# Performance work log

Hardware: AMD Instinct MI355X
Metric: run time of the kernel (lower is better)

Reference implementation:

```python
import jax, jax.numpy as jnp
import numpy as np

OUT_HW = 224  # fixed by the dilation tensor built inside forward
K = 3         # kernel size


def _axis_terms(coords, size):
    """Bilinear interpolation terms along one axis.
    coords: float coordinates, any shape. Returns clipped int neighbor
    indices (i0, i1) and weights (w0, w1) with zero weight outside [0, size)."""
    c0 = jnp.floor(coords)
    f = coords - c0
    i0 = c0.astype(jnp.int32)
    i1 = i0 + 1
    w0 = (1.0 - f) * ((i0 >= 0) & (i0 < size)).astype(coords.dtype)
    w1 = f * ((i1 >= 0) & (i1 < size)).astype(coords.dtype)
    return jnp.clip(i0, 0, size - 1), jnp.clip(i1, 0, size - 1), w0, w1


def setup_inputs() -> dict:
    key = jax.random.key(0)
    k1, k2, k3 = jax.random.split(key, 3)
    B, C, H, W = 16, 3, 1024, 1024
    x = jax.random.normal(k1, (B, C, H, W), dtype=jnp.float32)
    # normalized sample coordinates in [-1, 1] per output row / column
    stride_h = jax.random.uniform(k2, (B, OUT_HW), dtype=jnp.float32, minval=-1.0, maxval=1.0)
    stride_w = jax.random.uniform(k3, (B, OUT_HW), dtype=jnp.float32, minval=-1.0, maxval=1.0)
    # fixed identity weight from __init__: center tap on channel diagonal
    w = np.zeros((3, 3, K, K), dtype=np.float32)
    for c in range(3):
        w[c, c, 1, 1] = 1.0
    return {"x": x, "stride_h": stride_h, "stride_w": stride_w, "weight": jnp.asarray(w)}


def reference(x, stride_h, stride_w, weight):
    B, C, H, W = x.shape
    dt = x.dtype
    # map normalized [-1,1] coords to pixel coords (as in forward)
    ch = (stride_h + 1.0) * (H - 1) * 0.5            # [B, outH]
    cw = (stride_w + 1.0) * (W - 1) * 0.5            # [B, outW]
    offs = (jnp.arange(K, dtype=dt) - (K - 1) / 2)   # dilation == 1 (built as ones in forward)
    ys = ch[:, :, None] + offs                       # [B, outH, K]
    xs = cw[:, :, None] + offs                       # [B, outW, K]

    yi0, yi1, wy0, wy1 = _axis_terms(ys, H)
    xi0, xi1, wx0, wx1 = _axis_terms(xs, W)

    # gather rows: [B, C, outH, K, W]
    gat_h = jax.vmap(lambda xb, idx: xb[:, idx, :])
    row = (wy0[:, None, :, :, None] * gat_h(x, yi0)
           + wy1[:, None, :, :, None] * gat_h(x, yi1))
    # gather cols: [B, C, outH, Kh, outW, Kw]
    gat_w = jax.vmap(lambda rb, idx: rb[..., idx])
    samp = (wx0[:, None, None, None] * gat_w(row, xi0)
            + wx1[:, None, None, None] * gat_w(row, xi1))
    # contract with (fixed) kernel: out[b,o,i,j]
    return jnp.einsum('bciujv,ocuv->boij', samp, weight)
```

## Files before the change

### kernel.cpp

```cpp
#include <hip/hip_runtime.h>

#define OH 224
#define OW 224
#define HH 1024
#define WW 1024

typedef float f4u __attribute__((ext_vector_type(4), aligned(4)));

__global__ __launch_bounds__(256) void adaptive_sam_kernel(
    const float* __restrict__ x,
    const float* __restrict__ sh,
    const float* __restrict__ sw,
    const float* __restrict__ wgt,
    float* __restrict__ out,
    int B)
{
    __shared__ float ws[81];
    if (threadIdx.x < 81) ws[threadIdx.x] = wgt[threadIdx.x];
    __syncthreads();

    int site = blockIdx.x * blockDim.x + threadIdx.x;
    const int total = B * OH * OW;
    if (site >= total) return;

    int j = site % OW;
    int t = site / OW;
    int i = t % OH;
    int b = t / OH;

    float chf = (sh[b * OH + i] + 1.0f) * ((HH - 1) * 0.5f);
    float cwf = (sw[b * OW + j] + 1.0f) * ((WW - 1) * 0.5f);
    float cyf = floorf(chf); float fy = chf - cyf; int iy = (int)cyf;
    float cxf = floorf(cwf); float fx = cwf - cxf; int ix = (int)cxf;

    int rb = min(max(iy - 1, 0), HH - 4);
    int cb = min(max(ix - 1, 0), WW - 4);

    float Wy[3][4], Wx[3][4];
    #pragma unroll
    for (int u = 0; u < 3; ++u) {
        int y0 = iy + u - 1, y1 = y0 + 1;
        float a0 = (1.0f - fy) * ((y0 >= 0 && y0 < HH) ? 1.0f : 0.0f);
        float a1 = fy          * ((y1 >= 0 && y1 < HH) ? 1.0f : 0.0f);
        int py0 = min(max(y0, 0), HH - 1) - rb;
        int py1 = min(max(y1, 0), HH - 1) - rb;

        int x0 = ix + u - 1, x1 = x0 + 1;
        float b0 = (1.0f - fx) * ((x0 >= 0 && x0 < WW) ? 1.0f : 0.0f);
        float b1 = fx          * ((x1 >= 0 && x1 < WW) ? 1.0f : 0.0f);
        int px0 = min(max(x0, 0), WW - 1) - cb;
        int px1 = min(max(x1, 0), WW - 1) - cb;

        #pragma unroll
        for (int p = 0; p < 4; ++p) {
            Wy[u][p] = (py0 == p ? a0 : 0.0f) + (py1 == p ? a1 : 0.0f);
            Wx[u][p] = (px0 == p ? b0 : 0.0f) + (px1 == p ? b1 : 0.0f);
        }
    }

    float acc0 = 0.0f, acc1 = 0.0f, acc2 = 0.0f;
    const float* xb = x + (size_t)b * 3 * HH * WW;

    #pragma unroll
    for (int c = 0; c < 3; ++c) {
        const float* pr = xb + (size_t)c * HH * WW + (size_t)rb * WW + cb;
        f4u q0 = *reinterpret_cast<const f4u*>(pr);
        f4u q1 = *reinterpret_cast<const f4u*>(pr + WW);
        f4u q2 = *reinterpret_cast<const f4u*>(pr + 2 * WW);
        f4u q3 = *reinterpret_cast<const f4u*>(pr + 3 * WW);

        float hx[4][3];
        #pragma unroll
        for (int v = 0; v < 3; ++v) {
            hx[0][v] = Wx[v][0]*q0.x + Wx[v][1]*q0.y + Wx[v][2]*q0.z + Wx[v][3]*q0.w;
            hx[1][v] = Wx[v][0]*q1.x + Wx[v][1]*q1.y + Wx[v][2]*q1.z + Wx[v][3]*q1.w;
            hx[2][v] = Wx[v][0]*q2.x + Wx[v][1]*q2.y + Wx[v][2]*q2.z + Wx[v][3]*q2.w;
            hx[3][v] = Wx[v][0]*q3.x + Wx[v][1]*q3.y + Wx[v][2]*q3.z + Wx[v][3]*q3.w;
        }
        #pragma unroll
        for (int u = 0; u < 3; ++u)
            #pragma unroll
            for (int v = 0; v < 3; ++v) {
                float s = Wy[u][0]*hx[0][v] + Wy[u][1]*hx[1][v]
                        + Wy[u][2]*hx[2][v] + Wy[u][3]*hx[3][v];
                int wi = c * 9 + u * 3 + v;
                acc0 = fmaf(ws[wi],      s, acc0);
                acc1 = fmaf(ws[27 + wi], s, acc1);
                acc2 = fmaf(ws[54 + wi], s, acc2);
            }
    }

    size_t obase = (size_t)b * 3 * OH * OW + (size_t)i * OW + j;
    out[obase]               = acc0;
    out[obase + OH * OW]     = acc1;
    out[obase + 2 * OH * OW] = acc2;
}

extern "C" void kernel_launch(void* const* d_in, const int* in_sizes, int n_in,
                              void* d_out, int out_size, void* d_ws, size_t ws_size,
                              hipStream_t stream) {
    const float* x  = (const float*)d_in[0];
    const float* sh = (const float*)d_in[1];
    const float* sw = (const float*)d_in[2];
    const float* w  = (const float*)d_in[3];
    float* out = (float*)d_out;

    int B = in_sizes[1] / OH;
    int total = B * OH * OW;
    dim3 grid((total + 255) / 256);
    adaptive_sam_kernel<<<grid, 256, 0, stream>>>(x, sh, sw, w, out, B);
}
```

Baseline: 266.5 us.

## Stage four input rows per output row into LDS with async global_load_lds

The kernel now launches one block per (batch, output row). Each block copies the four needed input rows for all three channels into shared memory, 48KB, using coalesced 16-byte global_load_lds transfers. Threads then read their 4x4 neighbourhoods from LDS instead of doing scattered unaligned global float4 gathers. The aim is to turn random sub-line accesses into streaming contiguous loads. In exchange it always fetches full rows, even columns no thread uses, and the large LDS footprint limits how many blocks fit on a CU, with no overlap between the load and compute phases inside a block.

```diff
diff --git a/kernel.cpp b/kernel.cpp
--- a/kernel.cpp
+++ b/kernel.cpp
@@ -4,8 +4,10 @@
 #define OW 224
 #define HH 1024
 #define WW 1024
+#define HW (HH * WW)
 
-typedef float f4u __attribute__((ext_vector_type(4), aligned(4)));
+typedef __attribute__((address_space(3))) void lds_void_t;
+typedef const __attribute__((address_space(1))) void g_void_t;
 
 __global__ __launch_bounds__(256) void adaptive_sam_kernel(
     const float* __restrict__ x,
@@ -15,85 +17,97 @@
     float* __restrict__ out,
     int B)
 {
+    __shared__ float lds[3 * 4 * WW];
     __shared__ float ws[81];
-    if (threadIdx.x < 81) ws[threadIdx.x] = wgt[threadIdx.x];
+
+    const int tid = threadIdx.x;
+    const int bi  = blockIdx.x;
+    const int i   = bi % OH;
+    const int b   = bi / OH;
+
+    if (tid < 81) ws[tid] = wgt[tid];
+
+    float chf = (sh[b * OH + i] + 1.0f) * ((HH - 1) * 0.5f);
+    float cyf = floorf(chf); float fy = chf - cyf; int iy = (int)cyf;
+    int rb = min(max(iy - 1, 0), HH - 4);
+
+    {
+        const int lane = tid & 63;
+        const int wv   = tid >> 6;
+        #pragma unroll
+        for (int c = 0; c < 3; ++c) {
+            const float* gbase = x + (size_t)(b * 3 + c) * HW + (size_t)rb * WW + wv * 1024;
+            float* lbase = &lds[c * 4096 + wv * 1024];
+            #pragma unroll
+            for (int n = 0; n < 4; ++n) {
+                const float* gp = gbase + n * 256 + lane * 4;
+                __builtin_amdgcn_global_load_lds((g_void_t*)gp,
+                                                 (lds_void_t*)(lbase + n * 256),
+                                                 16, 0, 0);
+            }
+        }
+    }
     __syncthreads();
 
-    int site = blockIdx.x * blockDim.x + threadIdx.x;
-    const int total = B * OH * OW;
-    if (site >= total) return;
+    if (tid < OW) {
+        const int j = tid;
+        float cwf = (sw[b * OW + j] + 1.0f) * ((WW - 1) * 0.5f);
+        float cxf = floorf(cwf); float fx = cwf - cxf; int ix = (int)cxf;
+        int cb = min(max(ix - 1, 0), WW - 4);
 
-    int j = site % OW;
-    int t = site / OW;
-    int i = t % OH;
-    int b = t / OH;
+        float Wy[3][4], Wx[3][4];
+        #pragma unroll
+        for (int u = 0; u < 3; ++u) {
+            int y0 = iy + u - 1, y1 = y0 + 1;
+            float a0 = (1.0f - fy) * ((y0 >= 0 && y0 < HH) ? 1.0f : 0.0f);
+            float a1 = fy          * ((y1 >= 0 && y1 < HH) ? 1.0f : 0.0f);
+            int py0 = min(max(y0, 0), HH - 1) - rb;
+            int py1 = min(max(y1, 0), HH - 1) - rb;
 
-    float chf = (sh[b * OH + i] + 1.0f) * ((HH - 1) * 0.5f);
-    float cwf = (sw[b * OW + j] + 1.0f) * ((WW - 1) * 0.5f);
-    float cyf = floorf(chf); float fy = chf - cyf; int iy = (int)cyf;
-    float cxf = floorf(cwf); float fx = cwf - cxf; int ix = (int)cxf;
+            int x0 = ix + u - 1, x1 = x0 + 1;
+            float b0 = (1.0f - fx) * ((x0 >= 0 && x0 < WW) ? 1.0f : 0.0f);
+            float b1 = fx          * ((x1 >= 0 && x1 < WW) ? 1.0f : 0.0f);
+            int px0 = min(max(x0, 0), WW - 1) - cb;
+            int px1 = min(max(x1, 0), WW - 1) - cb;
 
-    int rb = min(max(iy - 1, 0), HH - 4);
-    int cb = min(max(ix - 1, 0), WW - 4);
+            #pragma unroll
+            for (int p = 0; p < 4; ++p) {
+                Wy[u][p] = (py0 == p ? a0 : 0.0f) + (py1 == p ? a1 : 0.0f);
+                Wx[u][p] = (px0 == p ? b0 : 0.0f) + (px1 == p ? b1 : 0.0f);
+            }
+        }
 
-    float Wy[3][4], Wx[3][4];
-    #pragma unroll
-    for (int u = 0; u < 3; ++u) {
-        int y0 = iy + u - 1, y1 = y0 + 1;
-        float a0 = (1.0f - fy) * ((y0 >= 0 && y0 < HH) ? 1.0f : 0.0f);
-        float a1 = fy          * ((y1 >= 0 && y1 < HH) ? 1.0f : 0.0f);
-        int py0 = min(max(y0, 0), HH - 1) - rb;
-        int py1 = min(max(y1, 0), HH - 1) - rb;
+        float acc0 = 0.0f, acc1 = 0.0f, acc2 = 0.0f;
+        #pragma unroll
+        for (int c = 0; c < 3; ++c) {
+            float hx[4][3];
+            #pragma unroll
+            for (int r = 0; r < 4; ++r) {
+                const float* lp = &lds[c * 4096 + r * 1024 + cb];
+                float p0 = lp[0], p1 = lp[1], p2 = lp[2], p3 = lp[3];
+                #pragma unroll
+                for (int v = 0; v < 3; ++v)
+                    hx[r][v] = Wx[v][0] * p0 + Wx[v][1] * p1
+                             + Wx[v][2] * p2 + Wx[v][3] * p3;
+            }
+            #pragma unroll
+            for (int u = 0; u < 3; ++u)
+                #pragma unroll
+                for (int v = 0; v < 3; ++v) {
+                    float s = Wy[u][0] * hx[0][v] + Wy[u][1] * hx[1][v]
+                            + Wy[u][2] * hx[2][v] + Wy[u][3] * hx[3][v];
+                    int wi = c * 9 + u * 3 + v;
+                    acc0 = fmaf(ws[wi],      s, acc0);
+                    acc1 = fmaf(ws[27 + wi], s, acc1);
+                    acc2 = fmaf(ws[54 + wi], s, acc2);
+                }
+        }
 
-        int x0 = ix + u - 1, x1 = x0 + 1;
-        float b0 = (1.0f - fx) * ((x0 >= 0 && x0 < WW) ? 1.0f : 0.0f);
-        float b1 = fx          * ((x1 >= 0 && x1 < WW) ? 1.0f : 0.0f);
-        int px0 = min(max(x0, 0), WW - 1) - cb;
-        int px1 = min(max(x1, 0), WW - 1) - cb;
-
-        #pragma unroll
-        for (int p = 0; p < 4; ++p) {
-            Wy[u][p] = (py0 == p ? a0 : 0.0f) + (py1 == p ? a1 : 0.0f);
-            Wx[u][p] = (px0 == p ? b0 : 0.0f) + (px1 == p ? b1 : 0.0f);
-        }
+        size_t obase = (size_t)b * 3 * OH * OW + (size_t)i * OW + j;
+        out[obase]                = acc0;
+        out[obase + OH * OW]      = acc1;
+        out[obase + 2 * OH * OW]  = acc2;
     }
-
-    float acc0 = 0.0f, acc1 = 0.0f, acc2 = 0.0f;
-    const float* xb = x + (size_t)b * 3 * HH * WW;
-
-    #pragma unroll
-    for (int c = 0; c < 3; ++c) {
-        const float* pr = xb + (size_t)c * HH * WW + (size_t)rb * WW + cb;
-        f4u q0 = *reinterpret_cast<const f4u*>(pr);
-        f4u q1 = *reinterpret_cast<const f4u*>(pr + WW);
-        f4u q2 = *reinterpret_cast<const f4u*>(pr + 2 * WW);
-        f4u q3 = *reinterpret_cast<const f4u*>(pr + 3 * WW);
-
-        float hx[4][3];
-        #pragma unroll
-        for (int v = 0; v < 3; ++v) {
-            hx[0][v] = Wx[v][0]*q0.x + Wx[v][1]*q0.y + Wx[v][2]*q0.z + Wx[v][3]*q0.w;
-            hx[1][v] = Wx[v][0]*q1.x + Wx[v][1]*q1.y + Wx[v][2]*q1.z + Wx[v][3]*q1.w;
-            hx[2][v] = Wx[v][0]*q2.x + Wx[v][1]*q2.y + Wx[v][2]*q2.z + Wx[v][3]*q2.w;
-            hx[3][v] = Wx[v][0]*q3.x + Wx[v][1]*q3.y + Wx[v][2]*q3.z + Wx[v][3]*q3.w;
-        }
-        #pragma unroll
-        for (int u = 0; u < 3; ++u)
-            #pragma unroll
-            for (int v = 0; v < 3; ++v) {
-                float s = Wy[u][0]*hx[0][v] + Wy[u][1]*hx[1][v]
-                        + Wy[u][2]*hx[2][v] + Wy[u][3]*hx[3][v];
-                int wi = c * 9 + u * 3 + v;
-                acc0 = fmaf(ws[wi],      s, acc0);
-                acc1 = fmaf(ws[27 + wi], s, acc1);
-                acc2 = fmaf(ws[54 + wi], s, acc2);
-            }
-    }
-
-    size_t obase = (size_t)b * 3 * OH * OW + (size_t)i * OW + j;
-    out[obase]               = acc0;
-    out[obase + OH * OW]     = acc1;
-    out[obase + 2 * OH * OW] = acc2;
 }
 
 extern "C" void kernel_launch(void* const* d_in, const int* in_sizes, int n_in,
@@ -106,7 +120,6 @@
     float* out = (float*)d_out;
 
     int B = in_sizes[1] / OH;
-    int total = B * OH * OW;
-    dim3 grid((total + 255) / 256);
+    dim3 grid(B * OH);
     adaptive_sam_kernel<<<grid, 256, 0, stream>>>(x, sh, sw, w, out, B);
 }
```

Result: no change. 263.1 us, median of 2 (-1.3%).
